# Kernel tuning notes

Hardware: AMD Instinct MI355X
Metric: run time of the kernel (lower is better)

Reference implementation:

```python
import jax, jax.numpy as jnp
import numpy as np

QWEN_H = 2048
SNN_H = 512


def setup_inputs() -> dict:
    key = jax.random.key(0)
    k0, k1, k2, k3, k4 = jax.random.split(key, 5)
    hidden_states = jax.random.normal(k0, (4, 2048, QWEN_H), dtype=jnp.float32)
    # nn.Linear weights stored as [out, in]
    w_down = jax.random.normal(k1, (SNN_H, QWEN_H), dtype=jnp.float32) / np.sqrt(QWEN_H)
    w_up = jax.random.normal(k2, (QWEN_H, SNN_H), dtype=jnp.float32) / np.sqrt(SNN_H)
    w1 = jax.random.normal(k3, (SNN_H, SNN_H), dtype=jnp.float32) / np.sqrt(SNN_H)
    w2 = jax.random.normal(k4, (SNN_H, SNN_H), dtype=jnp.float32) / np.sqrt(SNN_H)
    residual_scale = jnp.float32(0.1)
    return {"hidden_states": hidden_states, "w_down": w_down, "w_up": w_up,
            "w1": w1, "w2": w2, "residual_scale": residual_scale}


def reference(hidden_states, w_down, w_up, w1, w2, residual_scale):
    # Faithful math of SNNMiddleLayer.forward. The spike pulse encode ->
    # SpikeFP32Linear (fp32 accumulation) -> pulse decode path is a lossless
    # FP32 spike encoding of an ordinary bias-free linear layer, so the
    # per-timestep loop computes exactly out_t = w2 @ (w1 @ proj_down(x_t)),
    # which we express as fused batched GEMMs over all timesteps.
    residual = hidden_states
    x = jnp.einsum('bsq,hq->bsh', hidden_states, w_down)   # proj_down
    h = jnp.einsum('bsh,oh->bso', x, w1)                   # snn_linear1
    o = jnp.einsum('bso,po->bsp', h, w2)                   # snn_linear2
    out = jnp.einsum('bsp,qp->bsq', o, w_up)               # proj_up
    return residual + residual_scale * out
```

## Files before the change

kernel.cpp:

```cpp
#include <hip/hip_runtime.h>
#include <hip/hip_bf16.h>
#include <stdint.h>

using bf16 = __hip_bfloat16;
typedef __attribute__((ext_vector_type(8))) short bf16x8;
typedef __attribute__((ext_vector_type(4))) float f32x4;

__device__ __forceinline__ void async_load16(const void* g, void* l) {
    __builtin_amdgcn_global_load_lds(
        (__attribute__((address_space(1))) const void*)g,
        (__attribute__((address_space(3))) void*)l,
        16, 0, 0);
}

__device__ __forceinline__ void cvt_block_2048(const float* __restrict__ src,
                                               bf16* __restrict__ dst, int relblk) {
    int i = (relblk * 256 + (int)threadIdx.x) * 8;
    float4 f0 = *(const float4*)(src + i);
    float4 f1 = *(const float4*)(src + i + 4);
    union { bf16 h[8]; uint4 u; } o;
    o.h[0] = __float2bfloat16(f0.x); o.h[1] = __float2bfloat16(f0.y);
    o.h[2] = __float2bfloat16(f0.z); o.h[3] = __float2bfloat16(f0.w);
    o.h[4] = __float2bfloat16(f1.x); o.h[5] = __float2bfloat16(f1.y);
    o.h[6] = __float2bfloat16(f1.z); o.h[7] = __float2bfloat16(f1.w);
    *(uint4*)(dst + i) = o.u;
}

__global__ __launch_bounds__(256) void prep_w(
    const float* __restrict__ w1, bf16* __restrict__ w1b,
    const float* __restrict__ wup, bf16* __restrict__ wub,
    const float* __restrict__ wd, bf16* __restrict__ wdt,
    const float* __restrict__ w2, bf16* __restrict__ w2t) {
    __shared__ bf16 sh[32][33];
    int b = blockIdx.x;
    if (b < 128)       { cvt_block_2048(w1, w1b, b); return; }
    if (b < 640)       { cvt_block_2048(wup, wub, b - 128); return; }
    const float* src; bf16* dst; int R, C, tile, ntx;
    if (b < 1664) { src = wd; dst = wdt; R = 512; C = 2048; tile = b - 640; ntx = 64; }
    else          { src = w2; dst = w2t; R = 512; C = 512;  tile = b - 1664; ntx = 16; }
    const int bx = (tile % ntx) * 32, by = (tile / ntx) * 32;
    const int lx = threadIdx.x & 31;
    const int ly4 = ((int)threadIdx.x >> 5) * 4;
#pragma unroll
    for (int r = 0; r < 4; ++r)
        sh[ly4 + r][lx] = __float2bfloat16(src[(size_t)(by + ly4 + r) * C + bx + lx]);
    __syncthreads();
#pragma unroll
    for (int r = 0; r < 4; ++r)
        dst[(size_t)(bx + ly4 + r) * R + by + lx] = sh[lx][ly4 + r];
}

template<int BN, int NW>
__device__ __forceinline__ void stage_tiles(
    const bf16* __restrict__ A, const bf16* __restrict__ B,
    size_t bm, size_t bn, int K, int k0,
    bf16* __restrict__ As, bf16* __restrict__ Bs, int wave, int lane)
{
    const int srow = lane >> 3;
    const int scol = (lane & 7) ^ srow;
    constexpr int NCH = (128 + BN) / 8;
#pragma unroll
    for (int c = 0; c < NCH / NW; ++c) {
        const int cc = wave + c * NW;
        if (cc < 16) {
            const int rb = cc * 8;
            async_load16(A + (bm + rb + srow) * (size_t)K + k0 + scol * 8,
                         &As[rb * 64]);
        } else {
            const int rb = (cc - 16) * 8;
            async_load16(B + (bn + rb + srow) * (size_t)K + k0 + scol * 8,
                         &Bs[rb * 64]);
        }
    }
}

template<int BN, int EPI, int KT, int NW>
__device__ __forceinline__ void gemm_core(
    const bf16* __restrict__ A, const bf16* __restrict__ B,
    bf16* __restrict__ Cb, float* __restrict__ Cf,
    const float* __restrict__ Res, const float* __restrict__ sp,
    int N, int K, int bxi, int byi, bf16* smem)
{
    constexpr int BM = 128;
    constexpr int BK = 64;
    constexpr int WN = NW / 2;
    constexpr int NJ = 2;
    constexpr int BUF = (BM + BN) * BK;
    static_assert(BN == WN * 32, "wave tile is 64x32");
    static_assert(NW == 4 || NW == 8, "NW");
    static_assert(EPI == 0 || (NW == 8 && KT == 512), "EPI path: 8 waves, KT=512");

    const int tid  = threadIdx.x;
    const int wave = tid >> 6;
    const int lane = tid & 63;
    const int wm = wave / WN, wn = wave % WN;
    const size_t bm = (size_t)bxi * BM;
    const size_t bn = (size_t)byi * BN;

    f32x4 acc[4][NJ];
#pragma unroll
    for (int i = 0; i < 4; ++i)
#pragma unroll
        for (int j = 0; j < NJ; ++j)
            acc[i][j] = (f32x4){0.f, 0.f, 0.f, 0.f};

    float4 res_pre[EPI ? 8 : 1];
    const int r16 = lane >> 3;
    const int cbb = (lane & 7) * 4;

    auto compute_tile = [&](const bf16* Ap, const bf16* Bp) {
#pragma unroll
        for (int kk = 0; kk < 2; ++kk) {
            const int c8 = kk * 4 + (lane >> 4);
            bf16x8 af[4], bfr[NJ];
#pragma unroll
            for (int i = 0; i < 4; ++i) {
                const int r = wm * 64 + i * 16 + (lane & 15);
                af[i] = *(const bf16x8*)&Ap[(size_t)(r * 8 + (c8 ^ (r & 7))) * 8];
            }
#pragma unroll
            for (int j = 0; j < NJ; ++j) {
                const int r = wn * 32 + j * 16 + (lane & 15);
                bfr[j] = *(const bf16x8*)&Bp[(size_t)(r * 8 + (c8 ^ (r & 7))) * 8];
            }
#pragma unroll
            for (int i = 0; i < 4; ++i)
#pragma unroll
                for (int j = 0; j < NJ; ++j)
                    acc[i][j] = __builtin_amdgcn_mfma_f32_16x16x32_bf16(af[i], bfr[j], acc[i][j], 0, 0, 0);
        }
    };

    stage_tiles<BN, NW>(A, B, bm, bn, K, 0, smem, smem + BM * BK, wave, lane);
    __syncthreads();

    if constexpr (KT > 0) {
#pragma unroll
        for (int it = 0; it < KT / BK; ++it) {
            const int cur = it & 1;
            if (it + 1 < KT / BK) {
                bf16* nb = smem + (cur ^ 1) * BUF;
                stage_tiles<BN, NW>(A, B, bm, bn, KT, (it + 1) * BK, nb, nb + BM * BK, wave, lane);
            }
            if constexpr (EPI) {
                const int i = it >> 1, rh = it & 1;
                size_t row = bm + wm * 64 + i * 16 + rh * 8 + r16;
                size_t col = bn + wn * 32 + cbb;
                res_pre[it] = *(const float4*)&Res[row * (size_t)N + col];
            }
            const bf16* Ap = smem + cur * BUF;
            compute_tile(Ap, Ap + BM * BK);
            __syncthreads();
        }
    } else {
        int cur = 0;
        for (int k0 = 0; k0 < K; k0 += BK) {
            if (k0 + BK < K) {
                bf16* nb = smem + (cur ^ 1) * BUF;
                stage_tiles<BN, NW>(A, B, bm, bn, K, k0 + BK, nb, nb + BM * BK, wave, lane);
            }
            const bf16* Ap = smem + cur * BUF;
            compute_tile(Ap, Ap + BM * BK);
            __syncthreads();
            cur ^= 1;
        }
    }

    const int col_l = lane & 15;
    const int row_l = (lane >> 4) * 4;
    if (EPI == 0) {
#pragma unroll
        for (int i = 0; i < 4; ++i)
#pragma unroll
            for (int j = 0; j < NJ; ++j)
#pragma unroll
                for (int r = 0; r < 4; ++r) {
                    size_t row = bm + wm * 64 + i * 16 + row_l + r;
                    size_t col = bn + wn * 32 + j * 16 + col_l;
                    Cb[row * (size_t)N + col] = __float2bfloat16(acc[i][j][r]);
                }
    } else {
        const float s = *sp;
        float* lds_f = (float*)smem + wave * (16 * 36);
#pragma unroll
        for (int i = 0; i < 4; ++i) {
#pragma unroll
            for (int j = 0; j < NJ; ++j)
#pragma unroll
                for (int r = 0; r < 4; ++r)
                    lds_f[(row_l + r) * 36 + j * 16 + col_l] = acc[i][j][r];
#pragma unroll
            for (int rh = 0; rh < 2; ++rh) {
                const int rr = rh * 8 + r16;
                float4 v = *(float4*)&lds_f[rr * 36 + cbb];
                size_t row = bm + wm * 64 + i * 16 + rr;
                size_t col = bn + wn * 32 + cbb;
                size_t idx = row * (size_t)N + col;
                float4 rv = res_pre[i * 2 + rh];
                float4 o;
                o.x = rv.x + s * v.x; o.y = rv.y + s * v.y;
                o.z = rv.z + s * v.z; o.w = rv.w + s * v.w;
                *(float4*)&Cf[idx] = o;
            }
        }
    }
}

template<int BN, int EPI, int KT, int NW>
__global__ __launch_bounds__(NW * 64) void gemm_bf16(
    const bf16* __restrict__ A, const bf16* __restrict__ B,
    bf16* __restrict__ Cb, float* __restrict__ Cf,
    const float* __restrict__ Res, const float* __restrict__ sp, int N, int K) {
    __shared__ __align__(16) bf16 smem[(128 + BN) * 64 * 2];
    const int nx = gridDim.x;
    const int flat = blockIdx.y * nx + blockIdx.x;
    const int chunk = (nx * gridDim.y) >> 3;
    const int swz = (flat & 7) * chunk + (flat >> 3);
    gemm_core<BN, EPI, KT, NW>(A, B, Cb, Cf, Res, sp, N, K,
                               swz / nx, swz % nx, smem);
}

__global__ __launch_bounds__(256) void x_gemm(
    const float* __restrict__ A32, const bf16* __restrict__ B,
    bf16* __restrict__ Cb, int N, int K)
{
    constexpr int BM = 128, BN = 64, BK = 64;
    constexpr int BUF = (BM + BN) * BK;
    __shared__ __align__(16) bf16 smem[BUF * 2];

    const int nx = gridDim.x;
    const int flat = blockIdx.y * nx + blockIdx.x;
    const int chunk = (nx * gridDim.y) >> 3;
    const int swz = (flat & 7) * chunk + (flat >> 3);
    const int bxi = swz / nx, byi = swz % nx;
    const size_t bm = (size_t)bxi * BM;
    const size_t bn = (size_t)byi * BN;

    const int tid = threadIdx.x, wave = tid >> 6, lane = tid & 63;
    const int wm = wave >> 1, wn = wave & 1;

    f32x4 acc[4][2];
#pragma unroll
    for (int i = 0; i < 4; ++i)
#pragma unroll
        for (int j = 0; j < 2; ++j)
            acc[i][j] = (f32x4){0.f, 0.f, 0.f, 0.f};

    float4 av[4][2];

    auto loadA = [&](int k0) {
#pragma unroll
        for (int u = 0; u < 4; ++u) {
            const int unit = tid + u * 256;
            const int r = unit >> 3, c8 = unit & 7;
            const float* g = A32 + (bm + r) * (size_t)K + k0 + c8 * 8;
            av[u][0] = *(const float4*)g;
            av[u][1] = *(const float4*)(g + 4);
        }
    };
    auto writeA = [&](bf16* As) {
#pragma unroll
        for (int u = 0; u < 4; ++u) {
            const int unit = tid + u * 256;
            const int r = unit >> 3, c8 = unit & 7;
            const int su = (r >> 3) * 64 + (r & 7) * 8 + (c8 ^ (r & 7));
            union { bf16 h[8]; uint4 q; } o;
            o.h[0] = __float2bfloat16(av[u][0].x); o.h[1] = __float2bfloat16(av[u][0].y);
            o.h[2] = __float2bfloat16(av[u][0].z); o.h[3] = __float2bfloat16(av[u][0].w);
            o.h[4] = __float2bfloat16(av[u][1].x); o.h[5] = __float2bfloat16(av[u][1].y);
            o.h[6] = __float2bfloat16(av[u][1].z); o.h[7] = __float2bfloat16(av[u][1].w);
            *(uint4*)&As[(size_t)su * 8] = o.q;
        }
    };
    auto stageB = [&](bf16* Bs, int k0) {
        const int srow = lane >> 3;
        const int scol = (lane & 7) ^ srow;
#pragma unroll
        for (int c = 0; c < 2; ++c) {
            const int rb = (wave + c * 4) * 8;
            async_load16(B + (bn + rb + srow) * (size_t)K + k0 + scol * 8,
                         &Bs[rb * 64]);
        }
    };
    auto compute = [&](const bf16* Ap, const bf16* Bp) {
#pragma unroll
        for (int kk = 0; kk < 2; ++kk) {
            const int c8 = kk * 4 + (lane >> 4);
            bf16x8 af[4], bfr[2];
#pragma unroll
            for (int i = 0; i < 4; ++i) {
                const int r = wm * 64 + i * 16 + (lane & 15);
                af[i] = *(const bf16x8*)&Ap[(size_t)(r * 8 + (c8 ^ (r & 7))) * 8];
            }
#pragma unroll
            for (int j = 0; j < 2; ++j) {
                const int r = wn * 32 + j * 16 + (lane & 15);
                bfr[j] = *(const bf16x8*)&Bp[(size_t)(r * 8 + (c8 ^ (r & 7))) * 8];
            }
#pragma unroll
            for (int i = 0; i < 4; ++i)
#pragma unroll
                for (int j = 0; j < 2; ++j)
                    acc[i][j] = __builtin_amdgcn_mfma_f32_16x16x32_bf16(af[i], bfr[j], acc[i][j], 0, 0, 0);
        }
    };

    loadA(0);
    writeA(smem);
    stageB(smem + BM * BK, 0);
    __syncthreads();

    int cur = 0;
    for (int k0 = 0; k0 < K; k0 += BK) {
        const bool more = (k0 + BK) < K;
        if (more) {
            loadA(k0 + BK);
            stageB(smem + (cur ^ 1) * BUF + BM * BK, k0 + BK);
        }
        compute(smem + cur * BUF, smem + cur * BUF + BM * BK);
        if (more) writeA(smem + (cur ^ 1) * BUF);
        __syncthreads();
        cur ^= 1;
    }

    const int col_l = lane & 15;
    const int row_l = (lane >> 4) * 4;
#pragma unroll
    for (int i = 0; i < 4; ++i)
#pragma unroll
        for (int j = 0; j < 2; ++j)
#pragma unroll
            for (int r = 0; r < 4; ++r) {
                size_t row = bm + wm * 64 + i * 16 + row_l + r;
                size_t col = bn + wn * 32 + j * 16 + col_l;
                Cb[row * (size_t)N + col] = __float2bfloat16(acc[i][j][r]);
            }
}

__global__ __launch_bounds__(256) void ru(
    const bf16* __restrict__ A0, const bf16* __restrict__ B0, bf16* __restrict__ C0,
    const bf16* __restrict__ A1, const bf16* __restrict__ B1, bf16* __restrict__ C1) {
    __shared__ __align__(16) bf16 smem[(128 + 64) * 64 * 2];
    int b = blockIdx.x;
    if (b < 128)
        gemm_core<64, 0, 0, 4>(A0, B0, C0, nullptr, nullptr, nullptr, 2048, 512,
                               b / 32, b % 32, smem);
    else {
        int bb = b - 128;
        gemm_core<64, 0, 0, 4>(A1, B1, C1, nullptr, nullptr, nullptr, 512, 512,
                               bb / 8, bb % 8, smem);
    }
}

extern "C" void kernel_launch(void* const* d_in, const int* in_sizes, int n_in,
                              void* d_out, int out_size, void* d_ws, size_t ws_size,
                              hipStream_t stream) {
    const float* hs     = (const float*)d_in[0];
    const float* w_down = (const float*)d_in[1];
    const float* w_up   = (const float*)d_in[2];
    const float* w1     = (const float*)d_in[3];
    const float* w2     = (const float*)d_in[4];
    const float* rs     = (const float*)d_in[5];

    char* ws = (char*)d_ws;
    bf16* x_b   = (bf16*)(ws + 33554432);
    bf16* w1_b  = (bf16*)(ws + 41943040);
    bf16* wu_b  = (bf16*)(ws + 42467328);
    bf16* wdt_b = (bf16*)(ws + 44564480);
    bf16* w2t_b = (bf16*)(ws + 46661632);
    bf16* Rm    = (bf16*)(ws + 47185920);
    bf16* Um    = (bf16*)(ws + 49283072);

    prep_w<<<dim3(1920), dim3(256), 0, stream>>>(w1, w1_b, w_up, wu_b, w_down, wdt_b, w2, w2t_b);
    ru<<<dim3(256), dim3(256), 0, stream>>>(w1_b, wdt_b, Rm, wu_b, w2t_b, Um);
    x_gemm<<<dim3(8, 64), dim3(256), 0, stream>>>(hs, Rm, x_b, 512, 2048);
    gemm_bf16<128, 1, 512, 8><<<dim3(16, 64), dim3(512), 0, stream>>>(x_b, Um, nullptr, (float*)d_out,
                                                                      hs, rs, 2048, 512);
}
```

Baseline: 196.0 us.

## Stage fp32 A tile via async LDS loads, convert at fragment read, widen BN

The first GEMM (hidden_states times the fused down-projection) now copies the fp32 A tile straight into LDS with async global-to-LDS loads and an XOR swizzle. It converts to bf16 only when building MFMA fragments, instead of loading through registers, converting, and writing bf16 to LDS. The block tile widens to 128x128 with 512 threads, halving the grid and the number of times each A row is re-read from global memory. LDS use roughly doubles (96KB), which cuts occupancy, and the fp32 to bf16 conversion is now repeated by every N-wave that reads the same A rows.

```diff
diff --git a/kernel.cpp b/kernel.cpp
--- a/kernel.cpp
+++ b/kernel.cpp
@@ -220,13 +220,13 @@
                                swz / nx, swz % nx, smem);
 }
 
-__global__ __launch_bounds__(256) void x_gemm(
+__global__ __launch_bounds__(512) void x_gemm2f(
     const float* __restrict__ A32, const bf16* __restrict__ B,
     bf16* __restrict__ Cb, int N, int K)
 {
-    constexpr int BM = 128, BN = 64, BK = 64;
-    constexpr int BUF = (BM + BN) * BK;
-    __shared__ __align__(16) bf16 smem[BUF * 2];
+    constexpr int BM = 128, BN = 128, BK = 64;
+    constexpr int BUFB = 48 * 1024;
+    __shared__ __align__(16) char smem[BUFB * 2];
 
     const int nx = gridDim.x;
     const int flat = blockIdx.y * nx + blockIdx.x;
@@ -237,7 +237,7 @@
     const size_t bn = (size_t)byi * BN;
 
     const int tid = threadIdx.x, wave = tid >> 6, lane = tid & 63;
-    const int wm = wave >> 1, wn = wave & 1;
+    const int wm = wave >> 2, wn = wave & 3;
 
     f32x4 acc[4][2];
 #pragma unroll
@@ -246,43 +246,28 @@
         for (int j = 0; j < 2; ++j)
             acc[i][j] = (f32x4){0.f, 0.f, 0.f, 0.f};
 
-    float4 av[4][2];
-
-    auto loadA = [&](int k0) {
+    auto stage = [&](char* buf, int k0) {
+        float* Af = (float*)buf;
+        bf16*  Bs = (bf16*)(buf + 32768);
 #pragma unroll
         for (int u = 0; u < 4; ++u) {
-            const int unit = tid + u * 256;
-            const int r = unit >> 3, c8 = unit & 7;
-            const float* g = A32 + (bm + r) * (size_t)K + k0 + c8 * 8;
-            av[u][0] = *(const float4*)g;
-            av[u][1] = *(const float4*)(g + 4);
-        }
-    };
-    auto writeA = [&](bf16* As) {
-#pragma unroll
-        for (int u = 0; u < 4; ++u) {
-            const int unit = tid + u * 256;
-            const int r = unit >> 3, c8 = unit & 7;
-            const int su = (r >> 3) * 64 + (r & 7) * 8 + (c8 ^ (r & 7));
-            union { bf16 h[8]; uint4 q; } o;
-            o.h[0] = __float2bfloat16(av[u][0].x); o.h[1] = __float2bfloat16(av[u][0].y);
-            o.h[2] = __float2bfloat16(av[u][0].z); o.h[3] = __float2bfloat16(av[u][0].w);
-            o.h[4] = __float2bfloat16(av[u][1].x); o.h[5] = __float2bfloat16(av[u][1].y);
-            o.h[6] = __float2bfloat16(av[u][1].z); o.h[7] = __float2bfloat16(av[u][1].w);
-            *(uint4*)&As[(size_t)su * 8] = o.q;
-        }
-    };
-    auto stageB = [&](bf16* Bs, int k0) {
+            const int s = tid + u * 512;
+            const int r = s >> 4, sc = s & 15;
+            const int gc = sc ^ (2 * (r & 7));
+            async_load16(A32 + (bm + r) * (size_t)K + k0 + gc * 4, &Af[(size_t)s * 4]);
+        }
         const int srow = lane >> 3;
         const int scol = (lane & 7) ^ srow;
 #pragma unroll
         for (int c = 0; c < 2; ++c) {
-            const int rb = (wave + c * 4) * 8;
+            const int rb = (wave + c * 8) * 8;
             async_load16(B + (bn + rb + srow) * (size_t)K + k0 + scol * 8,
                          &Bs[rb * 64]);
         }
     };
-    auto compute = [&](const bf16* Ap, const bf16* Bp) {
+    auto compute = [&](const char* buf) {
+        const float* Af = (const float*)buf;
+        const bf16*  Bp = (const bf16*)(buf + 32768);
 #pragma unroll
         for (int kk = 0; kk < 2; ++kk) {
             const int c8 = kk * 4 + (lane >> 4);
@@ -290,7 +275,15 @@
 #pragma unroll
             for (int i = 0; i < 4; ++i) {
                 const int r = wm * 64 + i * 16 + (lane & 15);
-                af[i] = *(const bf16x8*)&Ap[(size_t)(r * 8 + (c8 ^ (r & 7))) * 8];
+                const float* src = &Af[(size_t)(r * 16 + 2 * (c8 ^ (r & 7))) * 4];
+                float4 f0 = *(const float4*)src;
+                float4 f1 = *(const float4*)(src + 4);
+                union { bf16 h[8]; bf16x8 v; } o;
+                o.h[0] = __float2bfloat16(f0.x); o.h[1] = __float2bfloat16(f0.y);
+                o.h[2] = __float2bfloat16(f0.z); o.h[3] = __float2bfloat16(f0.w);
+                o.h[4] = __float2bfloat16(f1.x); o.h[5] = __float2bfloat16(f1.y);
+                o.h[6] = __float2bfloat16(f1.z); o.h[7] = __float2bfloat16(f1.w);
+                af[i] = o.v;
             }
 #pragma unroll
             for (int j = 0; j < 2; ++j) {
@@ -305,20 +298,14 @@
         }
     };
 
-    loadA(0);
-    writeA(smem);
-    stageB(smem + BM * BK, 0);
+    stage(smem, 0);
     __syncthreads();
 
     int cur = 0;
     for (int k0 = 0; k0 < K; k0 += BK) {
-        const bool more = (k0 + BK) < K;
-        if (more) {
-            loadA(k0 + BK);
-            stageB(smem + (cur ^ 1) * BUF + BM * BK, k0 + BK);
-        }
-        compute(smem + cur * BUF, smem + cur * BUF + BM * BK);
-        if (more) writeA(smem + (cur ^ 1) * BUF);
+        if (k0 + BK < K)
+            stage(smem + (cur ^ 1) * BUFB, k0 + BK);
+        compute(smem + cur * BUFB);
         __syncthreads();
         cur ^= 1;
     }
@@ -373,7 +360,7 @@
 
     prep_w<<<dim3(1920), dim3(256), 0, stream>>>(w1, w1_b, w_up, wu_b, w_down, wdt_b, w2, w2t_b);
     ru<<<dim3(256), dim3(256), 0, stream>>>(w1_b, wdt_b, Rm, wu_b, w2t_b, Um);
-    x_gemm<<<dim3(8, 64), dim3(256), 0, stream>>>(hs, Rm, x_b, 512, 2048);
+    x_gemm2f<<<dim3(4, 64), dim3(512), 0, stream>>>(hs, Rm, x_b, 512, 2048);
     gemm_bf16<128, 1, 512, 8><<<dim3(16, 64), dim3(512), 0, stream>>>(x_b, Um, nullptr, (float*)d_out,
                                                                       hs, rs, 2048, 512);
 }
```

New measurement: 258.2 us. 31.8% more time.
